# Performance work log

Hardware: AMD Instinct MI355X
Metric: run time of the kernel (lower is better)

Reference implementation:

```python
import jax, jax.numpy as jnp
import numpy as np

N = 100_000   # nodes
E = 1_250_000 # edges
D = 64        # feature dim


def setup_inputs() -> dict:
    key = jax.random.key(0)
    k1, k2, k3, k4 = jax.random.split(key, 4)
    x = jax.random.normal(k1, (N, D), dtype=jnp.float32)
    edge_index = jax.random.randint(k2, (2, E), 0, N, dtype=jnp.int32)
    s = 1.0 / np.sqrt(D)  # glorot-ish scale
    W1 = jax.random.uniform(k3, (D, D), minval=-s, maxval=s, dtype=jnp.float32)
    W2 = jax.random.uniform(k4, (D, D), minval=-s, maxval=s, dtype=jnp.float32)
    b1 = jnp.zeros((D,), jnp.float32)
    b2 = jnp.zeros((D,), jnp.float32)
    return {"x": x, "edge_index": edge_index, "W1": W1, "b1": b1, "W2": W2, "b2": b2}


def gcn_conv(x, edge_index, W, b):
    # PyG GCNConv: add self-loops, symmetric normalization D^-1/2 A D^-1/2,
    # linear transform, scatter-add aggregation over destination nodes.
    n = x.shape[0]
    src, dst = edge_index[0], edge_index[1]
    xw = x @ W  # [N, D]
    deg = jax.ops.segment_sum(jnp.ones((edge_index.shape[1],), x.dtype), dst,
                              num_segments=n) + 1.0  # +1 for self-loop
    inv_sqrt = jax.lax.rsqrt(deg)  # [N]
    coef = inv_sqrt[src] * inv_sqrt[dst]  # [E]
    agg = jax.ops.segment_sum(xw[src] * coef[:, None], dst, num_segments=n)
    # self-loop contribution: coef_ii = deg_i^-1
    agg = agg + xw * (inv_sqrt * inv_sqrt)[:, None]
    return agg + b


def reference(x, edge_index, W1, b1, W2, b2):
    h = jax.nn.relu(gcn_conv(x, edge_index, W1, b1))
    # dropout p=0.6 is identity in eval mode (training=False)
    out = gcn_conv(h, edge_index, W2, b2)
    return jax.nn.log_softmax(out, axis=1)
```

## Files before the change

kernel.cpp:

```cpp
#include <hip/hip_runtime.h>

#define DD 64
#define BSH 8
#define NB_MAX 512
#define SCAP 4096
#define BIN_CH 4096

typedef __attribute__((ext_vector_type(8))) short bf16x8;
typedef __attribute__((ext_vector_type(4))) float f32x4;
union Frag { bf16x8 v; uint32_t d[4]; };

__device__ __forceinline__ float bf_lo(uint32_t d) { return __uint_as_float(d << 16); }
__device__ __forceinline__ float bf_hi(uint32_t d) { return __uint_as_float(d & 0xffff0000u); }
__device__ __forceinline__ float bf2f(uint32_t h) { return __uint_as_float(h << 16); }
__device__ __forceinline__ uint32_t f2bf(float f) {
    uint32_t u = __float_as_uint(f);
    u += 0x7fffu + ((u >> 16) & 1u);
    return u >> 16;
}

__global__ __launch_bounds__(256) void bin_kernel(const int* __restrict__ src,
                                                  const int* __restrict__ dst,
                                                  int* __restrict__ bcnt,
                                                  uint32_t* __restrict__ staging,
                                                  int E, int NB) {
    __shared__ uint32_t cnt[NB_MAX];
    __shared__ uint32_t resv[NB_MAX];
    __shared__ uint16_t rk[BIN_CH];
    int tid = threadIdx.x;
    int base = blockIdx.x * BIN_CH;
    for (int b = tid; b < NB; b += 256) cnt[b] = 0;
    __syncthreads();
    for (int k = tid; k < BIN_CH; k += 256) {
        int g = base + k;
        if (g < E) {
            int b = dst[g] >> BSH;
            rk[k] = (uint16_t)atomicAdd(&cnt[b], 1u);
        }
    }
    __syncthreads();
    for (int b = tid; b < NB; b += 256) {
        uint32_t c = cnt[b];
        resv[b] = c ? (uint32_t)atomicAdd(&bcnt[b], (int)c) : 0u;
    }
    __syncthreads();
    for (int k = tid; k < BIN_CH; k += 256) {
        int g = base + k;
        if (g < E) {
            int s = src[g], d = dst[g];
            int b = d >> BSH;
            uint32_t pos = resv[b] + rk[k];
            if (pos < SCAP)
                staging[(size_t)b * SCAP + pos] = ((uint32_t)s << BSH) | (uint32_t)(d & ((1 << BSH) - 1));
        }
    }
}

__global__ __launch_bounds__(256) void sort_kernel(const int* __restrict__ bcnt,
                                                   const uint32_t* __restrict__ staging,
                                                   int* __restrict__ rowptr,
                                                   float* __restrict__ inv,
                                                   uint32_t* __restrict__ srcs,
                                                   int n, int E, int NB) {
    __shared__ uint32_t raw[SCAP];
    __shared__ uint32_t sorted[SCAP];
    __shared__ int scnt[1 << BSH];
    __shared__ int soff[1 << BSH];
    __shared__ int lcur[1 << BSH];
    __shared__ int red[256];
    int tid = threadIdx.x;
    int b = blockIdx.x;
    int base = b << BSH;
    int nd = min(1 << BSH, n - base);
    int cb = min(bcnt[b], SCAP);

    int part = 0;
    for (int j = tid; j < b; j += 256) part += bcnt[j];
    red[tid] = part;
    __syncthreads();
    for (int o = 128; o > 0; o >>= 1) {
        if (tid < o) red[tid] += red[tid + o];
        __syncthreads();
    }
    int bbase = red[0];

    scnt[tid] = 0;
    if (tid < ((1 << BSH) - 256)) {}
    __syncthreads();
    for (int k = tid; k < cb; k += 256) {
        uint32_t w = staging[(size_t)b * SCAP + k];
        raw[k] = w;
        atomicAdd(&scnt[w & ((1 << BSH) - 1)], 1);
    }
    __syncthreads();
    int v = scnt[tid];
    red[tid] = v;
    __syncthreads();
    for (int o = 1; o < 256; o <<= 1) {
        int t = (tid >= o) ? red[tid - o] : 0;
        __syncthreads();
        red[tid] += t;
        __syncthreads();
    }
    soff[tid] = red[tid] - v;
    lcur[tid] = red[tid] - v;
    if (tid < nd) {
        rowptr[base + tid] = bbase + soff[tid];
        inv[base + tid] = rsqrtf((float)v + 1.0f);
    }
    if (b == NB - 1 && tid == 0) rowptr[n] = E;
    __syncthreads();
    for (int k = tid; k < cb; k += 256) {
        uint32_t w = raw[k];
        int p = atomicAdd(&lcur[w & ((1 << BSH) - 1)], 1);
        sorted[p] = w >> BSH;
    }
    __syncthreads();
    for (int k = tid; k < cb; k += 256) srcs[bbase + k] = sorted[k];
}

template <int XBF>
__global__ __launch_bounds__(256) void gemm64_mfma(const void* __restrict__ Xv,
                                                   const float* __restrict__ W,
                                                   const float* __restrict__ inv,
                                                   uint16_t* __restrict__ Y, int n) {
    __shared__ float Ws[DD * DD];
    int tid = threadIdx.x;
    for (int i = tid; i < DD * DD; i += 256) Ws[i] = W[i];
    __syncthreads();
    int lane = tid & 63, quad = lane >> 4, l16 = lane & 15;

    Frag bhi[4][2], blo[4][2];
#pragma unroll
    for (int t = 0; t < 4; ++t)
#pragma unroll
        for (int c = 0; c < 2; ++c) {
            int col = t * 16 + l16;
            int kb = c * 32 + quad * 8;
#pragma unroll
            for (int i = 0; i < 4; ++i) {
                float w0 = Ws[(kb + 2 * i) * DD + col];
                float w1 = Ws[(kb + 2 * i + 1) * DD + col];
                uint32_t h0 = f2bf(w0), h1 = f2bf(w1);
                uint32_t l0 = f2bf(w0 - bf2f(h0)), l1 = f2bf(w1 - bf2f(h1));
                bhi[t][c].d[i] = h0 | (h1 << 16);
                blo[t][c].d[i] = l0 | (l1 << 16);
            }
        }

    int ngroups = (n + 15) >> 4;
    int nwaves = gridDim.x * 4;
    int wid = blockIdx.x * 4 + (tid >> 6);
    for (int g = wid; g < ngroups; g += nwaves) {
        int rb = g << 4;
        int row = min(rb + l16, n - 1);
        f32x4 acc[4];
#pragma unroll
        for (int t = 0; t < 4; ++t) acc[t] = (f32x4){0.f, 0.f, 0.f, 0.f};
#pragma unroll
        for (int c = 0; c < 2; ++c) {
            Frag ahi, alo;
            if constexpr (XBF == 0) {
                const float* xr = (const float*)Xv + (size_t)row * DD + c * 32 + quad * 8;
                float4 x0 = *(const float4*)xr;
                float4 x1 = *(const float4*)(xr + 4);
                float f[8] = {x0.x, x0.y, x0.z, x0.w, x1.x, x1.y, x1.z, x1.w};
#pragma unroll
                for (int i = 0; i < 4; ++i) {
                    uint32_t h0 = f2bf(f[2 * i]), h1 = f2bf(f[2 * i + 1]);
                    ahi.d[i] = h0 | (h1 << 16);
                    alo.d[i] = f2bf(f[2 * i] - bf2f(h0)) | (f2bf(f[2 * i + 1] - bf2f(h1)) << 16);
                }
            } else {
                const int4* xr = (const int4*)((const uint32_t*)Xv + (size_t)row * 32 + c * 16 + quad * 4);
                int4 a = *xr;
                ahi.d[0] = a.x; ahi.d[1] = a.y; ahi.d[2] = a.z; ahi.d[3] = a.w;
            }
#pragma unroll
            for (int t = 0; t < 4; ++t) {
                acc[t] = __builtin_amdgcn_mfma_f32_16x16x32_bf16(ahi.v, bhi[t][c].v, acc[t], 0, 0, 0);
                acc[t] = __builtin_amdgcn_mfma_f32_16x16x32_bf16(ahi.v, blo[t][c].v, acc[t], 0, 0, 0);
                if constexpr (XBF == 0)
                    acc[t] = __builtin_amdgcn_mfma_f32_16x16x32_bf16(alo.v, bhi[t][c].v, acc[t], 0, 0, 0);
            }
        }
#pragma unroll
        for (int r = 0; r < 4; ++r) {
            int ro = rb + quad * 4 + r;
            if (ro < n) {
                float sc = inv[ro];
#pragma unroll
                for (int t = 0; t < 4; ++t)
                    Y[(size_t)ro * DD + t * 16 + l16] = (uint16_t)f2bf(acc[t][r] * sc);
            }
        }
    }
}

template <int MODE>
__global__ __launch_bounds__(256) void agg_kernel(const int* __restrict__ rowptr,
                                                  const uint32_t* __restrict__ srcs,
                                                  const float* __restrict__ inv,
                                                  const uint32_t* __restrict__ XWb,
                                                  const float* __restrict__ b,
                                                  void* __restrict__ OUTv, int n) {
    int gid = blockIdx.x * 256 + threadIdx.x;
    int i = gid >> 6, lane = gid & 63;
    if (i >= n) return;
    int g = lane >> 3, m = lane & 7;

    float a[8];
#pragma unroll
    for (int k = 0; k < 8; ++k) a[k] = 0.f;
    if (g == 0) {
        int4 d = *(const int4*)(XWb + (size_t)i * 32 + 4 * m);
        a[0] = bf_lo((uint32_t)d.x); a[1] = bf_hi((uint32_t)d.x);
        a[2] = bf_lo((uint32_t)d.y); a[3] = bf_hi((uint32_t)d.y);
        a[4] = bf_lo((uint32_t)d.z); a[5] = bf_hi((uint32_t)d.z);
        a[6] = bf_lo((uint32_t)d.w); a[7] = bf_hi((uint32_t)d.w);
    }

    int jstart = rowptr[i], jend = rowptr[i + 1];
    if (jstart < jend) {
        int last = jend - 1;
        int jq = jstart + g;
        uint32_t s0 = srcs[min(jq, last)];
        uint32_t s1 = srcs[min(jq + 8, last)];
        uint32_t s2 = srcs[min(jq + 16, last)];
        int4 d0 = *(const int4*)(XWb + (size_t)s0 * 32 + 4 * m);
        int4 d1 = *(const int4*)(XWb + (size_t)s1 * 32 + 4 * m);
        for (int j = jq; j < jend; j += 8) {
            uint32_t s3 = srcs[min(j + 24, last)];
            int4 d2 = *(const int4*)(XWb + (size_t)s2 * 32 + 4 * m);
            a[0] += bf_lo((uint32_t)d0.x); a[1] += bf_hi((uint32_t)d0.x);
            a[2] += bf_lo((uint32_t)d0.y); a[3] += bf_hi((uint32_t)d0.y);
            a[4] += bf_lo((uint32_t)d0.z); a[5] += bf_hi((uint32_t)d0.z);
            a[6] += bf_lo((uint32_t)d0.w); a[7] += bf_hi((uint32_t)d0.w);
            s2 = s3;
            d0 = d1; d1 = d2;
        }
    }

#pragma unroll
    for (int k = 0; k < 8; ++k) {
        a[k] += __shfl_xor(a[k], 8, 64);
        a[k] += __shfl_xor(a[k], 16, 64);
        a[k] += __shfl_xor(a[k], 32, 64);
    }

    float iv = inv[i];
    float4 bb0 = *(const float4*)(b + 8 * m);
    float4 bb1 = *(const float4*)(b + 8 * m + 4);
    float f0 = fmaf(a[0], iv, bb0.x), f1 = fmaf(a[1], iv, bb0.y);
    float f2 = fmaf(a[2], iv, bb0.z), f3 = fmaf(a[3], iv, bb0.w);
    float f4 = fmaf(a[4], iv, bb1.x), f5 = fmaf(a[5], iv, bb1.y);
    float f6 = fmaf(a[6], iv, bb1.z), f7 = fmaf(a[7], iv, bb1.w);

    if (MODE == 0) {
        if (g == 0) {
            int4 d;
            d.x = (int)((f2bf(fmaxf(f1, 0.f)) << 16) | f2bf(fmaxf(f0, 0.f)));
            d.y = (int)((f2bf(fmaxf(f3, 0.f)) << 16) | f2bf(fmaxf(f2, 0.f)));
            d.z = (int)((f2bf(fmaxf(f5, 0.f)) << 16) | f2bf(fmaxf(f4, 0.f)));
            d.w = (int)((f2bf(fmaxf(f7, 0.f)) << 16) | f2bf(fmaxf(f6, 0.f)));
            *(int4*)((uint32_t*)OUTv + (size_t)i * 32 + 4 * m) = d;
        }
    } else {
        float mx = fmaxf(fmaxf(fmaxf(f0, f1), fmaxf(f2, f3)),
                         fmaxf(fmaxf(f4, f5), fmaxf(f6, f7)));
#pragma unroll
        for (int o = 4; o > 0; o >>= 1) mx = fmaxf(mx, __shfl_xor(mx, o, 64));
        float e = __expf(f0 - mx) + __expf(f1 - mx) + __expf(f2 - mx) + __expf(f3 - mx)
                + __expf(f4 - mx) + __expf(f5 - mx) + __expf(f6 - mx) + __expf(f7 - mx);
#pragma unroll
        for (int o = 4; o > 0; o >>= 1) e += __shfl_xor(e, o, 64);
        float ls = __logf(e);
        if (g == 0) {
            float4 r0 = make_float4(f0 - mx - ls, f1 - mx - ls, f2 - mx - ls, f3 - mx - ls);
            float4 r1 = make_float4(f4 - mx - ls, f5 - mx - ls, f6 - mx - ls, f7 - mx - ls);
            *(float4*)((float*)OUTv + (size_t)i * DD + 8 * m) = r0;
            *(float4*)((float*)OUTv + (size_t)i * DD + 8 * m + 4) = r1;
        }
    }
}

extern "C" void kernel_launch(void* const* d_in, const int* in_sizes, int n_in,
                              void* d_out, int out_size, void* d_ws, size_t ws_size,
                              hipStream_t stream) {
    const float* x  = (const float*)d_in[0];
    const int*   ei = (const int*)d_in[1];
    const float* W1 = (const float*)d_in[2];
    const float* b1 = (const float*)d_in[3];
    const float* W2 = (const float*)d_in[4];
    const float* b2 = (const float*)d_in[5];
    float* out = (float*)d_out;

    const int n = in_sizes[0] / DD;
    const int E = in_sizes[1] / 2;
    const int* src = ei;
    const int* dst = ei + E;
    const int NB = (n + (1 << BSH) - 1) >> BSH;

    size_t off = 0;
    int* base = (int*)d_ws;
    int* bcnt = base + off; off += NB_MAX;
    uint32_t* staging = (uint32_t*)(base + off); off += (size_t)NB_MAX * SCAP;
    uint32_t* srcs = (uint32_t*)(base + off); off += E;
    int* rowptr = base + off; off += (size_t)n + 1;
    float* inv  = (float*)(base + off); off += n;
    uint32_t* XWb = (uint32_t*)(base + off); off += (size_t)n * 32;
    uint32_t* hb  = (uint32_t*)(base + off); off += (size_t)n * 32;

    hipMemsetAsync(bcnt, 0, NB_MAX * sizeof(int), stream);
    bin_kernel<<<(E + BIN_CH - 1) / BIN_CH, 256, 0, stream>>>(src, dst, bcnt, staging, E, NB);
    sort_kernel<<<NB, 256, 0, stream>>>(bcnt, staging, rowptr, inv, srcs, n, E, NB);

    gemm64_mfma<0><<<1024, 256, 0, stream>>>(x, W1, inv, (uint16_t*)XWb, n);
    agg_kernel<0><<<(n * DD + 255) / 256, 256, 0, stream>>>(rowptr, srcs, inv, XWb, b1, hb, n);

    gemm64_mfma<1><<<1024, 256, 0, stream>>>(hb, W2, inv, (uint16_t*)XWb, n);
    agg_kernel<1><<<(n * DD + 255) / 256, 256, 0, stream>>>(rowptr, srcs, inv, XWb, b2, out, n);
}
```

Baseline: 246.4 us.

## Process two nodes per wavefront in aggregation and pre-scale source indices

The aggregation kernel now maps each 64-lane wavefront to two destination nodes (32 lanes each, 4 edge groups) instead of one node with 8 edge groups. This cuts lane waste on low-degree rows and shortens the cross-group shuffle reduction, while the prefetch pipeline is deepened to three in-flight rows. Source indices are stored pre-shifted by 5 so the gather address needs no multiply. GEMM launch size now follows n rather than a fixed 1024 blocks, which could change GEMM occupancy or its grid-stride behaviour.

```diff
diff --git a/kernel.cpp b/kernel.cpp
--- a/kernel.cpp
+++ b/kernel.cpp
@@ -85,7 +85,6 @@
     int bbase = red[0];
 
     scnt[tid] = 0;
-    if (tid < ((1 << BSH) - 256)) {}
     __syncthreads();
     for (int k = tid; k < cb; k += 256) {
         uint32_t w = staging[(size_t)b * SCAP + k];
@@ -116,7 +115,7 @@
         sorted[p] = w >> BSH;
     }
     __syncthreads();
-    for (int k = tid; k < cb; k += 256) srcs[bbase + k] = sorted[k];
+    for (int k = tid; k < cb; k += 256) srcs[bbase + k] = sorted[k] << 5;
 }
 
 template <int XBF>
@@ -205,39 +204,46 @@
                                                   const float* __restrict__ b,
                                                   void* __restrict__ OUTv, int n) {
     int gid = blockIdx.x * 256 + threadIdx.x;
-    int i = gid >> 6, lane = gid & 63;
-    if (i >= n) return;
-    int g = lane >> 3, m = lane & 7;
+    int w = gid >> 6, lane = gid & 63;
+    if (w * 2 >= n) return;
+    int h = lane >> 5, l = lane & 31;
+    int i = w * 2 + h;
+    bool act = i < n;
+    int ic = act ? i : n - 1;
+    int g = l >> 3, m = l & 7;
 
     float a[8];
 #pragma unroll
     for (int k = 0; k < 8; ++k) a[k] = 0.f;
     if (g == 0) {
-        int4 d = *(const int4*)(XWb + (size_t)i * 32 + 4 * m);
+        int4 d = *(const int4*)(XWb + (size_t)ic * 32 + 4 * m);
         a[0] = bf_lo((uint32_t)d.x); a[1] = bf_hi((uint32_t)d.x);
         a[2] = bf_lo((uint32_t)d.y); a[3] = bf_hi((uint32_t)d.y);
         a[4] = bf_lo((uint32_t)d.z); a[5] = bf_hi((uint32_t)d.z);
         a[6] = bf_lo((uint32_t)d.w); a[7] = bf_hi((uint32_t)d.w);
     }
 
-    int jstart = rowptr[i], jend = rowptr[i + 1];
+    int jstart = rowptr[ic];
+    int jend = act ? rowptr[ic + 1] : jstart;
     if (jstart < jend) {
         int last = jend - 1;
         int jq = jstart + g;
         uint32_t s0 = srcs[min(jq, last)];
-        uint32_t s1 = srcs[min(jq + 8, last)];
-        uint32_t s2 = srcs[min(jq + 16, last)];
-        int4 d0 = *(const int4*)(XWb + (size_t)s0 * 32 + 4 * m);
-        int4 d1 = *(const int4*)(XWb + (size_t)s1 * 32 + 4 * m);
-        for (int j = jq; j < jend; j += 8) {
-            uint32_t s3 = srcs[min(j + 24, last)];
-            int4 d2 = *(const int4*)(XWb + (size_t)s2 * 32 + 4 * m);
+        uint32_t s1 = srcs[min(jq + 4, last)];
+        uint32_t s2 = srcs[min(jq + 8, last)];
+        uint32_t s3 = srcs[min(jq + 12, last)];
+        int4 d0 = *(const int4*)(XWb + s0 + 4 * m);
+        int4 d1 = *(const int4*)(XWb + s1 + 4 * m);
+        int4 d2 = *(const int4*)(XWb + s2 + 4 * m);
+        for (int j = jq; j < jend; j += 4) {
+            uint32_t s4 = srcs[min(j + 16, last)];
+            int4 d3 = *(const int4*)(XWb + s3 + 4 * m);
             a[0] += bf_lo((uint32_t)d0.x); a[1] += bf_hi((uint32_t)d0.x);
             a[2] += bf_lo((uint32_t)d0.y); a[3] += bf_hi((uint32_t)d0.y);
             a[4] += bf_lo((uint32_t)d0.z); a[5] += bf_hi((uint32_t)d0.z);
             a[6] += bf_lo((uint32_t)d0.w); a[7] += bf_hi((uint32_t)d0.w);
-            s2 = s3;
-            d0 = d1; d1 = d2;
+            s3 = s4;
+            d0 = d1; d1 = d2; d2 = d3;
         }
     }
 
@@ -245,10 +251,9 @@
     for (int k = 0; k < 8; ++k) {
         a[k] += __shfl_xor(a[k], 8, 64);
         a[k] += __shfl_xor(a[k], 16, 64);
-        a[k] += __shfl_xor(a[k], 32, 64);
-    }
-
-    float iv = inv[i];
+    }
+
+    float iv = inv[ic];
     float4 bb0 = *(const float4*)(b + 8 * m);
     float4 bb1 = *(const float4*)(b + 8 * m + 4);
     float f0 = fmaf(a[0], iv, bb0.x), f1 = fmaf(a[1], iv, bb0.y);
@@ -257,7 +262,7 @@
     float f6 = fmaf(a[6], iv, bb1.z), f7 = fmaf(a[7], iv, bb1.w);
 
     if (MODE == 0) {
-        if (g == 0) {
+        if (act && g == 0) {
             int4 d;
             d.x = (int)((f2bf(fmaxf(f1, 0.f)) << 16) | f2bf(fmaxf(f0, 0.f)));
             d.y = (int)((f2bf(fmaxf(f3, 0.f)) << 16) | f2bf(fmaxf(f2, 0.f)));
@@ -275,7 +280,7 @@
 #pragma unroll
         for (int o = 4; o > 0; o >>= 1) e += __shfl_xor(e, o, 64);
         float ls = __logf(e);
-        if (g == 0) {
+        if (act && g == 0) {
             float4 r0 = make_float4(f0 - mx - ls, f1 - mx - ls, f2 - mx - ls, f3 - mx - ls);
             float4 r1 = make_float4(f4 - mx - ls, f5 - mx - ls, f6 - mx - ls, f7 - mx - ls);
             *(float4*)((float*)OUTv + (size_t)i * DD + 8 * m) = r0;
@@ -315,9 +320,13 @@
     bin_kernel<<<(E + BIN_CH - 1) / BIN_CH, 256, 0, stream>>>(src, dst, bcnt, staging, E, NB);
     sort_kernel<<<NB, 256, 0, stream>>>(bcnt, staging, rowptr, inv, srcs, n, E, NB);
 
-    gemm64_mfma<0><<<1024, 256, 0, stream>>>(x, W1, inv, (uint16_t*)XWb, n);
-    agg_kernel<0><<<(n * DD + 255) / 256, 256, 0, stream>>>(rowptr, srcs, inv, XWb, b1, hb, n);
-
-    gemm64_mfma<1><<<1024, 256, 0, stream>>>(hb, W2, inv, (uint16_t*)XWb, n);
-    agg_kernel<1><<<(n * DD + 255) / 256, 256, 0, stream>>>(rowptr, srcs, inv, XWb, b2, out, n);
-}
+    const int ngroups = (n + 15) >> 4;
+    const int gblocks = (ngroups + 3) / 4;
+    const int ablocks = (n + 7) / 8;
+
+    gemm64_mfma<0><<<gblocks, 256, 0, stream>>>(x, W1, inv, (uint16_t*)XWb, n);
+    agg_kernel<0><<<ablocks, 256, 0, stream>>>(rowptr, srcs, inv, XWb, b1, hb, n);
+
+    gemm64_mfma<1><<<gblocks, 256, 0, stream>>>(hb, W2, inv, (uint16_t*)XWb, n);
+    agg_kernel<1><<<ablocks, 256, 0, stream>>>(rowptr, srcs, inv, XWb, b2, out, n);
+}
```

Measured after the change: 241.4 us. -2.0%, faster.
